# Kernel tuning notes

Hardware: AMD Instinct MI355X
Metric: run time of the kernel (lower is better)

## Reference

```python
import jax, jax.numpy as jnp
import numpy as np

N, T, NC, D = 256, 20, 1, 32
NF, Q, VSTEPS, HDYN = 16, 32, 10, 256
HDIM = NF * 64           # n_filt * 4**3
DT = 0.1
BETA = 1.0
LOG2PI = float(np.log(2.0 * np.pi))


def conv2d(x, w, b):
    # k=4, s=2, p=1 : halves spatial dims. x: [B,Cin,H,W], w: [Cout,Cin,4,4]
    y = jax.lax.conv_general_dilated(x, w, (2, 2), [(1, 1), (1, 1)],
                                     dimension_numbers=('NCHW', 'OIHW', 'NCHW'))
    return y + b[None, :, None, None]


def deconv2d(x, w, b):
    # stride-2 transposed conv, doubles spatial dims. w: [Cout,Cin,4,4]
    y = jax.lax.conv_transpose(x, w, (2, 2), 'SAME',
                               dimension_numbers=('NCHW', 'OIHW', 'NCHW'))
    return y + b[None, :, None, None]


def encode(x, C1, c1, C2, c2, C3, c3, Wm, bm, Wl, bl):
    h = jax.nn.relu(conv2d(x, C1, c1))
    h = jax.nn.relu(conv2d(h, C2, c2))
    h = jax.nn.relu(conv2d(h, C3, c3))   # [B, 4*NF, 4, 4]
    h = h.reshape(h.shape[0], -1)        # [B, HDIM]
    return h @ Wm + bm, h @ Wl + bl


def setup_inputs() -> dict:
    key = jax.random.key(0)
    ks = jax.random.split(key, 40)
    r = lambda i, shape, s=0.05: s * jax.random.normal(ks[i], shape, jnp.float32)
    inp = {
        'X': jax.random.uniform(ks[0], (N, T, NC, D, D), jnp.float32),
        'eps_s0': jax.random.normal(ks[1], (N, Q), jnp.float32),
        'eps_v0': jax.random.normal(ks[2], (N, Q), jnp.float32),
        # enc_s (input = 1 frame)
        'Cs1': r(3, (NF, NC, 4, 4)), 'cs1': jnp.zeros((NF,)),
        'Cs2': r(4, (2 * NF, NF, 4, 4)), 'cs2': jnp.zeros((2 * NF,)),
        'Cs3': r(5, (4 * NF, 2 * NF, 4, 4)), 'cs3': jnp.zeros((4 * NF,)),
        'Wsm': r(6, (HDIM, Q)), 'bsm': jnp.zeros((Q,)),
        'Wsl': r(7, (HDIM, Q), 0.01), 'bsl': -1.0 * jnp.ones((Q,)),
        # enc_v (input = v_steps frames stacked as channels)
        'Cv1': r(8, (NF, VSTEPS * NC, 4, 4)), 'cv1': jnp.zeros((NF,)),
        'Cv2': r(9, (2 * NF, NF, 4, 4)), 'cv2': jnp.zeros((2 * NF,)),
        'Cv3': r(10, (4 * NF, 2 * NF, 4, 4)), 'cv3': jnp.zeros((4 * NF,)),
        'Wvm': r(11, (HDIM, Q)), 'bvm': jnp.zeros((Q,)),
        'Wvl': r(12, (HDIM, Q), 0.01), 'bvl': -1.0 * jnp.ones((Q,)),
        # dynamics f : R^{2q} -> R^q (tanh MLP)
        'W1': r(13, (2 * Q, HDYN), 0.1), 'b1': jnp.zeros((HDYN,)),
        'W2': r(14, (HDYN, Q), 0.1), 'b2': jnp.zeros((Q,)),
        # fc3 + decoder
        'Wf': r(15, (Q, HDIM)), 'bf': jnp.zeros((HDIM,)),
        'D1': r(16, (2 * NF, 4 * NF, 4, 4)), 'd1': jnp.zeros((2 * NF,)),
        'D2': r(17, (NF, 2 * NF, 4, 4)), 'd2': jnp.zeros((NF,)),
        'D3': r(18, (NC, NF, 4, 4)), 'd3': jnp.zeros((NC,)),
        'Ndata': 10000,
    }
    return inp


def reference(X, eps_s0, eps_v0,
              Cs1, cs1, Cs2, cs2, Cs3, cs3, Wsm, bsm, Wsl, bsl,
              Cv1, cv1, Cv2, cv2, Cv3, cv3, Wvm, bvm, Wvl, bvl,
              W1, b1, W2, b2, Wf, bf, D1, d1, D2, d2, D3, d3, Ndata):
    Nb, Tt = X.shape[0], X.shape[1]
    # ---- encode z0 = [v0, s0]
    s0_mu, s0_lv = encode(X[:, 0], Cs1, cs1, Cs2, cs2, Cs3, cs3, Wsm, bsm, Wsl, bsl)
    xv = X[:, :VSTEPS].reshape(Nb, VSTEPS * NC, D, D)
    v0_mu, v0_lv = encode(xv, Cv1, cv1, Cv2, cv2, Cv3, cv3, Wvm, bvm, Wvl, bvl)
    s0 = s0_mu + eps_s0 * jnp.exp(s0_lv)
    v0 = v0_mu + eps_v0 * jnp.exp(v0_lv)
    # standard-normal density of the base noise (q dims each)
    logp0 = (-0.5 * jnp.sum(eps_s0 ** 2, -1) - 0.5 * Q * LOG2PI) + \
            (-0.5 * jnp.sum(eps_v0 ** 2, -1) - 0.5 * Q * LOG2PI)
    z0 = jnp.concatenate([v0, s0], axis=1)               # [N,2q]
    qz0_m = jnp.concatenate([v0_mu, s0_mu], axis=1)
    qz0_logv = jnp.concatenate([v0_lv, s0_lv], axis=1)

    # ---- augmented ODE rhs: dz = [f(z), v], dlogp = -tr(df/dv)
    # exact trace for the tanh MLP: J = W2^T diag(1-h^2) W1^T, so
    # tr_{i<q} J = (1-h^2) @ c with c_k = sum_{i<q} W1[i,k] * W2[k,i]
    c = jnp.sum(W1[:Q] * W2.T, axis=0)                   # [HDYN]

    def rhs(vs):
        h = jnp.tanh(vs @ W1 + b1)                       # [N,HDYN]
        dv = h @ W2 + b2                                 # [N,q]
        dvs = jnp.concatenate([dv, vs[:, :Q]], axis=1)   # [N,2q]
        tr = (1.0 - h * h) @ c                           # [N]
        return dvs, -tr

    def rk4_step(carry, _):
        z, lp = carry
        k1z, k1l = rhs(z)
        k2z, k2l = rhs(z + 0.5 * DT * k1z)
        k3z, k3l = rhs(z + 0.5 * DT * k2z)
        k4z, k4l = rhs(z + DT * k3z)
        z2 = z + (DT / 6.0) * (k1z + 2 * k2z + 2 * k3z + k4z)
        lp2 = lp + (DT / 6.0) * (k1l + 2 * k2l + 2 * k3l + k4l)
        return (z2, lp2), (z2, lp2)

    (_, _), (zs, lps) = jax.lax.scan(rk4_step, (z0, logp0), None, length=Tt - 1)
    zt = jnp.concatenate([z0[None], zs], axis=0)         # [T,N,2q]
    logp = jnp.concatenate([logp0[None], lps], axis=0)   # [T,N]
    ztL = jnp.transpose(zt, (1, 0, 2))[None]             # [1,N,T,2q] (L=1)
    logpL = logp.T[None]                                 # [1,N,T]

    # ---- decode positions s_t
    s = ztL[..., Q:].reshape(-1, Q) @ Wf + bf            # [N*T, HDIM]
    h = s.reshape(-1, 4 * NF, 4, 4)
    h = jax.nn.relu(deconv2d(h, D1, d1))                 # [N*T,2NF,8,8]
    h = jax.nn.relu(deconv2d(h, D2, d2))                 # [N*T,NF,16,16]
    Xrec = jax.nn.sigmoid(deconv2d(h, D3, d3))           # [N*T,NC,32,32]
    Xrec = Xrec.reshape(1, Nb, Tt, NC, D, D)

    # ---- ELBO
    log_pzt = -0.5 * jnp.sum(ztL ** 2, -1) - Q * LOG2PI  # N(0,I) over 2q dims
    kl_z = (logpL - log_pzt).sum(2).mean(0)              # [N]
    lhood_L = jnp.log(0.001 + Xrec) * X[None] + jnp.log(1.001 - Xrec) * (1.0 - X[None])
    lhood = lhood_L.sum((2, 3, 4, 5)).mean(0)            # [N]
    kl_w = 0.5 * (jnp.sum(W1 ** 2) + jnp.sum(W2 ** 2))
    Nd = jnp.float32(Ndata)
    lh = Nd * lhood.mean()
    klz = Nd * kl_z.mean()
    elbo = lh - klz - BETA * kl_w
    return Xrec, qz0_m, qz0_logv, ztL, elbo, lh, klz, BETA * kl_w


if __name__ == '__main__':
    outs = reference(**setup_inputs())
    print(outs[0].shape, float(outs[4]))
```

## Files before the change

kernel.cpp:

```cpp
#include <hip/hip_runtime.h>
#include <math.h>

#define N_S 256
#define T_S 20
#define D_S 32
#define NF_S 16
#define Q_S 32
#define HDYN_S 256
#define HDIM_S 1024
#define VSTEPS_S 10
#define DT_S 0.1f
#define LOG2PI_F 1.8378770664093453f

#define OUT_XREC 0
#define OUT_QM   5242880
#define OUT_QLV  5259264
#define OUT_ZT   5275648
#define OUT_SCAL 5603328

#define WS_A1    0
#define WS_A3    0
#define WS_A2    1048576
#define WS_S0MU  1572864
#define WS_S0LV  1581056
#define WS_V0MU  1589248
#define WS_V0LV  1597440
#define WS_LHOOD 1610752
#define WS_KLZ   1611008
#define WS_TC    1611520
#define TC_S1 (WS_TC + 0)
#define TC_V1 (WS_TC + 256)
#define TC_S2 (WS_TC + 2816)
#define TC_V2 (WS_TC + 11008)
#define TC_S3 (WS_TC + 19200)
#define TC_V3 (WS_TC + 51968)
#define WS_WT1   1703936
#define WS_WT2   1736704
#define WS_WT3   1744896
#define SC_A1S 0
#define SC_A2S 1048576
#define SC_A3S 1572864

__device__ inline void enc_tr(const float* __restrict__ src, float* __restrict__ dst,
                              int e, int CI, int CO) {
    int co = e % CO; int r = e / CO; int tap = r & 15; int ci = r >> 4;
    dst[e] = src[(co * CI + ci) * 16 + tap];
}
__device__ inline void dec_tr(const float* __restrict__ src, float* __restrict__ dst,
                              int e, int CI, int CO) {
    int co = e % CO; int r = e / CO; int ci = r % CI; int tap = r / CI;
    dst[e] = src[(co * CI + ci) * 16 + tap];
}

__global__ __launch_bounds__(256) void prep_all(
    const float* __restrict__ Cs1, const float* __restrict__ Cv1,
    const float* __restrict__ Cs2, const float* __restrict__ Cv2,
    const float* __restrict__ Cs3, const float* __restrict__ Cv3,
    const float* __restrict__ D1, const float* __restrict__ D2,
    const float* __restrict__ D3,
    float* __restrict__ ws)
{
    int idx = blockIdx.x * 256 + threadIdx.x;
    if (blockIdx.x == 0) ws[WS_LHOOD + threadIdx.x] = 0.f;
    if (idx < 256)        enc_tr(Cs1, ws + TC_S1, idx,          1, 16);
    else if (idx < 2816)  enc_tr(Cv1, ws + TC_V1, idx - 256,   10, 16);
    else if (idx < 11008) enc_tr(Cs2, ws + TC_S2, idx - 2816,  16, 32);
    else if (idx < 19200) enc_tr(Cv2, ws + TC_V2, idx - 11008, 16, 32);
    else if (idx < 51968) enc_tr(Cs3, ws + TC_S3, idx - 19200, 32, 64);
    else if (idx < 84736) enc_tr(Cv3, ws + TC_V3, idx - 51968, 32, 64);
    else if (idx < 117504) dec_tr(D1, ws + WS_WT1, idx - 84736,  64, 32);
    else if (idx < 125696) dec_tr(D2, ws + WS_WT2, idx - 117504, 32, 16);
    else if (idx < 125952) dec_tr(D3, ws + WS_WT3, idx - 125696, 16, 1);
}

__global__ __launch_bounds__(256) void conv1_both(
    const float* __restrict__ x,
    const float* __restrict__ wtS, const float* __restrict__ wtV,
    const float* __restrict__ bS, const float* __restrict__ bV,
    float* __restrict__ outS, float* __restrict__ outV)
{
    __shared__ float xin[10 * 630];
    __shared__ float wlv[10 * 256];
    __shared__ float wls[256];
    __shared__ float blv[16], bls[16];
    int b = blockIdx.x, yh = blockIdx.y, t = threadIdx.x;
    for (int e = t; e < 10 * 576; e += 256) {
        int ci = e / 576;
        int r = (e >> 5) - ci * 18;
        int cx = e & 31;
        int gy = yh * 16 - 1 + r;
        float v = (gy >= 0 && gy < 32) ? x[(size_t)b * 20480 + ci * 1024 + gy * 32 + cx] : 0.f;
        xin[ci * 630 + r * 35 + cx + 1] = v;
    }
    for (int e = t; e < 10 * 18; e += 256) {
        int ci = e / 18, r = e - ci * 18;
        xin[ci * 630 + r * 35 + 0] = 0.f;
        xin[ci * 630 + r * 35 + 33] = 0.f;
    }
    for (int e = t; e < 10 * 256; e += 256) wlv[e] = wtV[e];
    wls[t] = wtS[t];
    if (t < 16) { blv[t] = bV[t]; bls[t] = bS[t]; }
    __syncthreads();

    int ocq = t >> 7, p = t & 127;
    int oyl = p >> 4, ox = p & 15;
    float accv[8], accs[8];
    #pragma unroll
    for (int j = 0; j < 8; j++) { accv[j] = blv[ocq * 8 + j]; accs[j] = bls[ocq * 8 + j]; }
    for (int ci = 0; ci < 10; ci++) {
        const float* xc = xin + ci * 630;
        const float* wc = wlv + ci * 256 + ocq * 8;
        const float* wcs = wls + ocq * 8;
        bool do_s = (ci == 0);
        #pragma unroll
        for (int ky = 0; ky < 4; ky++) {
            const float* xr = xc + (2 * oyl + ky) * 35;
            #pragma unroll
            for (int kx = 0; kx < 4; kx++) {
                float v = xr[2 * ox + kx];
                const float4* w4 = (const float4*)(wc + (ky * 4 + kx) * 16);
                float4 wa = w4[0], wb = w4[1];
                accv[0] = fmaf(v, wa.x, accv[0]);
                accv[1] = fmaf(v, wa.y, accv[1]);
                accv[2] = fmaf(v, wa.z, accv[2]);
                accv[3] = fmaf(v, wa.w, accv[3]);
                accv[4] = fmaf(v, wb.x, accv[4]);
                accv[5] = fmaf(v, wb.y, accv[5]);
                accv[6] = fmaf(v, wb.z, accv[6]);
                accv[7] = fmaf(v, wb.w, accv[7]);
                if (do_s) {
                    const float4* s4 = (const float4*)(wcs + (ky * 4 + kx) * 16);
                    float4 sa = s4[0], sb = s4[1];
                    accs[0] = fmaf(v, sa.x, accs[0]);
                    accs[1] = fmaf(v, sa.y, accs[1]);
                    accs[2] = fmaf(v, sa.z, accs[2]);
                    accs[3] = fmaf(v, sa.w, accs[3]);
                    accs[4] = fmaf(v, sb.x, accs[4]);
                    accs[5] = fmaf(v, sb.y, accs[5]);
                    accs[6] = fmaf(v, sb.z, accs[6]);
                    accs[7] = fmaf(v, sb.w, accs[7]);
                }
            }
        }
    }
    int oy = yh * 8 + oyl;
    size_t ob = (size_t)b * 4096 + (size_t)(ocq * 8) * 256 + oy * 16 + ox;
    #pragma unroll
    for (int j = 0; j < 8; j++) {
        outV[ob + (size_t)j * 256] = fmaxf(accv[j], 0.f);
        outS[ob + (size_t)j * 256] = fmaxf(accs[j], 0.f);
    }
}

__global__ __launch_bounds__(256) void conv2_m(
    const float* __restrict__ a1S, const float* __restrict__ a1V,
    const float* __restrict__ wtS, const float* __restrict__ wtV,
    const float* __restrict__ bS, const float* __restrict__ bV,
    float* __restrict__ outS, float* __restrict__ outV)
{
    __shared__ float xin[16 * 272];
    __shared__ float wl[4096];
    __shared__ float bl[16];
    int b = blockIdx.x, h = blockIdx.y, z = blockIdx.z, t = threadIdx.x;
    const float* a1 = z ? a1V : a1S;
    const float* wt = z ? wtV : wtS;
    const float* bias = z ? bV : bS;
    float* out = z ? outV : outS;
    for (int e = t; e < 4096; e += 256) {
        int ci = e >> 8, r = e & 255, iy = r >> 4, ix = r & 15;
        xin[ci * 272 + iy * 17 + ix] = a1[(size_t)b * 4096 + e];
    }
    for (int e = t; e < 4096; e += 256) {
        int ci = e >> 8, r = e & 255, tap = r >> 4, oc = r & 15;
        wl[e] = wt[ci * 512 + tap * 32 + h * 16 + oc];
    }
    if (t < 16) bl[t] = bias[h * 16 + t];
    __syncthreads();

    int ocq = t >> 6, p = t & 63;
    int pa = p >> 3, pb = p & 7;
    float acc[4];
    #pragma unroll
    for (int j = 0; j < 4; j++) acc[j] = bl[ocq * 4 + j];
    for (int ci = 0; ci < 16; ci++) {
        const float* xc = xin + ci * 272;
        const float* wc = wl + ci * 256 + ocq * 4;
        #pragma unroll
        for (int ky = 0; ky < 4; ky++) {
            int iy = 2 * pa - 1 + ky;
            if ((unsigned)iy >= 16u) continue;
            const float* xr = xc + iy * 17;
            #pragma unroll
            for (int kx = 0; kx < 4; kx++) {
                int ix = 2 * pb - 1 + kx;
                if ((unsigned)ix >= 16u) continue;
                float v = xr[ix];
                float4 wv = *(const float4*)(wc + (ky * 4 + kx) * 16);
                acc[0] = fmaf(v, wv.x, acc[0]);
                acc[1] = fmaf(v, wv.y, acc[1]);
                acc[2] = fmaf(v, wv.z, acc[2]);
                acc[3] = fmaf(v, wv.w, acc[3]);
            }
        }
    }
    size_t ob = (size_t)b * 2048 + (size_t)(h * 16 + ocq * 4) * 64 + pa * 8 + pb;
    #pragma unroll
    for (int j = 0; j < 4; j++) out[ob + (size_t)j * 64] = fmaxf(acc[j], 0.f);
}

__global__ __launch_bounds__(256) void conv3_m(
    const float* __restrict__ a2S, const float* __restrict__ a2V,
    const float* __restrict__ wtS, const float* __restrict__ wtV,
    const float* __restrict__ bS, const float* __restrict__ bV,
    float* __restrict__ outS, float* __restrict__ outV)
{
    __shared__ float xin[32 * 72];
    __shared__ float wl[8192];
    __shared__ float bl[16];
    int b = blockIdx.x, h = blockIdx.y, z = blockIdx.z, t = threadIdx.x;
    const float* a2 = z ? a2V : a2S;
    const float* wt = z ? wtV : wtS;
    const float* bias = z ? bV : bS;
    float* out = z ? outV : outS;
    for (int e = t; e < 2048; e += 256) {
        int ci = e >> 6, r = e & 63, iy = r >> 3, ix = r & 7;
        xin[ci * 72 + iy * 9 + ix] = a2[(size_t)b * 2048 + e];
    }
    for (int e = t; e < 8192; e += 256) {
        int ci = e >> 8, r = e & 255, tap = r >> 4, oc = r & 15;
        wl[e] = wt[ci * 1024 + tap * 64 + h * 16 + oc];
    }
    if (t < 16) bl[t] = bias[h * 16 + t];
    __syncthreads();

    int oc = t >> 4, p = t & 15;
    int pa = p >> 2, pb = p & 3;
    float s0 = bl[oc], s1 = 0.f;
    for (int ci = 0; ci < 32; ci += 2) {
        const float* xc0 = xin + ci * 72;
        const float* wc0 = wl + ci * 256 + oc;
        #pragma unroll
        for (int ky = 0; ky < 4; ky++) {
            int iy = 2 * pa - 1 + ky;
            if ((unsigned)iy >= 8u) continue;
            const float* xr0 = xc0 + iy * 9;
            #pragma unroll
            for (int kx = 0; kx < 4; kx++) {
                int ix = 2 * pb - 1 + kx;
                if ((unsigned)ix >= 8u) continue;
                int wi = (ky * 4 + kx) * 16;
                s0 = fmaf(xr0[ix],      wc0[wi],       s0);
                s1 = fmaf(xr0[72 + ix], wc0[256 + wi], s1);
            }
        }
    }
    out[(size_t)b * 1024 + h * 256 + t] = fmaxf(s0 + s1, 0.f);
}

__global__ __launch_bounds__(256) void fc_m(
    const float* __restrict__ hS, const float* __restrict__ hV,
    const float* __restrict__ WsmP, const float* __restrict__ bsmP,
    const float* __restrict__ WslP, const float* __restrict__ bslP,
    const float* __restrict__ WvmP, const float* __restrict__ bvmP,
    const float* __restrict__ WvlP, const float* __restrict__ bvlP,
    float* __restrict__ muS, float* __restrict__ lvS,
    float* __restrict__ muV, float* __restrict__ lvV)
{
    __shared__ float pm[8][32], pl[8][32];
    int b = blockIdx.x, z = blockIdx.y, t = threadIdx.x;
    const float* h  = z ? hV : hS;
    const float* Wm = z ? WvmP : WsmP;
    const float* Wl = z ? WvlP : WslP;
    const float* bm = z ? bvmP : bsmP;
    const float* bl = z ? bvlP : bslP;
    float* mu = z ? muV : muS;
    float* lv = z ? lvV : lvS;
    int q = t & 31, c = t >> 5;
    const float* hb = h + (size_t)b * HDIM_S + c * 128;
    const float* wmp = Wm + (c * 128) * Q_S + q;
    const float* wlp = Wl + (c * 128) * Q_S + q;
    float am = 0.f, al = 0.f;
    #pragma unroll 4
    for (int k = 0; k < 128; k++) {
        float hv = hb[k];
        am = fmaf(hv, wmp[k * Q_S], am);
        al = fmaf(hv, wlp[k * Q_S], al);
    }
    pm[c][q] = am; pl[c][q] = al;
    __syncthreads();
    if (t < 32) {
        float s = bm[t];
        #pragma unroll
        for (int c2 = 0; c2 < 8; c2++) s += pm[c2][t];
        mu[b * Q_S + t] = s;
    } else if (t < 64) {
        int qq = t - 32;
        float s = bl[qq];
        #pragma unroll
        for (int c2 = 0; c2 < 8; c2++) s += pl[c2][qq];
        lv[b * Q_S + qq] = s;
    }
}

__global__ __launch_bounds__(256) void ode2(
    const float* __restrict__ W1, const float* __restrict__ b1,
    const float* __restrict__ W2, const float* __restrict__ b2,
    const float* __restrict__ s0mu, const float* __restrict__ s0lv,
    const float* __restrict__ v0mu, const float* __restrict__ v0lv,
    const float* __restrict__ eps_s, const float* __restrict__ eps_v,
    float* __restrict__ qm, float* __restrict__ qlv,
    float* __restrict__ ztL, float* __restrict__ klz)
{
    __shared__ float W2s[HDYN_S * Q_S];
    __shared__ float zeval[64];
    __shared__ float hsh[HDYN_S];
    __shared__ float dvred[HDYN_S];
    __shared__ float red4[4];
    int n = blockIdx.x;
    int t = threadIdx.x;

    for (int i = t; i < HDYN_S * Q_S; i += 256) W2s[i] = W2[i];
    float w1r[64];
    #pragma unroll
    for (int j = 0; j < 64; j++) w1r[j] = W1[j * HDYN_S + t];
    float b1r = b1[t];

    size_t zoff = (size_t)n * T_S * 64;
    float zj = 0.f, zevalj = 0.f, lp = 0.f, klzacc = 0.f;
    float ep = 0.f;
    if (t < 64) {
        int q = t & 31;
        float mu, lvv;
        if (t < 32) { mu = v0mu[n*32+q]; lvv = v0lv[n*32+q]; ep = eps_v[n*32+q]; }
        else        { mu = s0mu[n*32+q]; lvv = s0lv[n*32+q]; ep = eps_s[n*32+q]; }
        zj = fmaf(ep, expf(lvv), mu);
        qm[n*64 + t]  = mu;
        qlv[n*64 + t] = lvv;
        ztL[zoff + t] = zj;
        zevalj = zj; zeval[t] = zj;
        float e2 = ep * ep;
        float z2 = zj * zj;
        #pragma unroll
        for (int off = 32; off; off >>= 1) {
            e2 += __shfl_down(e2, off, 64);
            z2 += __shfl_down(z2, off, 64);
        }
        if (t == 0) {
            lp = -0.5f * e2 - Q_S * LOG2PI_F;
            klzacc = lp + 0.5f * z2 + Q_S * LOG2PI_F;
        }
    }
    __syncthreads();
    float ck = 0.f;
    #pragma unroll
    for (int i = 0; i < Q_S; i++) ck = fmaf(w1r[i], W2s[t * Q_S + i], ck);

    float ksumj = 0.f, lsum = 0.f;
    const float wc[4] = {1.f, 2.f, 2.f, 1.f};
    const float ac[3] = {0.5f * DT_S, 0.5f * DT_S, DT_S};

    for (int step = 1; step < T_S; step++) {
        for (int e = 0; e < 4; e++) {
            __syncthreads();
            float p0 = 0.f, p1 = 0.f, p2 = 0.f, p3 = 0.f;
            const float4* ze4 = (const float4*)zeval;
            #pragma unroll
            for (int jj = 0; jj < 4; jj++) {
                float4 za = ze4[jj], zb = ze4[jj + 4], zc = ze4[jj + 8], zd = ze4[jj + 12];
                p0 = fmaf(za.x, w1r[jj*4+0], p0);
                p0 = fmaf(za.y, w1r[jj*4+1], p0);
                p0 = fmaf(za.z, w1r[jj*4+2], p0);
                p0 = fmaf(za.w, w1r[jj*4+3], p0);
                p1 = fmaf(zb.x, w1r[16+jj*4+0], p1);
                p1 = fmaf(zb.y, w1r[16+jj*4+1], p1);
                p1 = fmaf(zb.z, w1r[16+jj*4+2], p1);
                p1 = fmaf(zb.w, w1r[16+jj*4+3], p1);
                p2 = fmaf(zc.x, w1r[32+jj*4+0], p2);
                p2 = fmaf(zc.y, w1r[32+jj*4+1], p2);
                p2 = fmaf(zc.z, w1r[32+jj*4+2], p2);
                p2 = fmaf(zc.w, w1r[32+jj*4+3], p2);
                p3 = fmaf(zd.x, w1r[48+jj*4+0], p3);
                p3 = fmaf(zd.y, w1r[48+jj*4+1], p3);
                p3 = fmaf(zd.z, w1r[48+jj*4+2], p3);
                p3 = fmaf(zd.w, w1r[48+jj*4+3], p3);
            }
            float pre = b1r + ((p0 + p1) + (p2 + p3));
            float hk = tanhf(pre);
            hsh[t] = hk;
            float gk = (1.f - hk * hk) * ck;
            #pragma unroll
            for (int off = 32; off; off >>= 1) gk += __shfl_down(gk, off, 64);
            if ((t & 63) == 0) red4[t >> 6] = gk;
            __syncthreads();
            {
                int i = t & 31, p = t >> 5;
                const float4* h4 = (const float4*)(hsh + p * 32);
                const float* wbase = W2s + (p * 32) * Q_S + i;
                float a0 = 0.f, a1 = 0.f;
                #pragma unroll
                for (int k4 = 0; k4 < 4; k4++) {
                    float4 ha = h4[k4], hb = h4[k4 + 4];
                    const float* wk = wbase + k4 * 4 * Q_S;
                    a0 = fmaf(ha.x, wk[0],        a0);
                    a0 = fmaf(ha.y, wk[Q_S],      a0);
                    a0 = fmaf(ha.z, wk[2*Q_S],    a0);
                    a0 = fmaf(ha.w, wk[3*Q_S],    a0);
                    const float* wk2 = wbase + (16 + k4 * 4) * Q_S;
                    a1 = fmaf(hb.x, wk2[0],       a1);
                    a1 = fmaf(hb.y, wk2[Q_S],     a1);
                    a1 = fmaf(hb.z, wk2[2*Q_S],   a1);
                    a1 = fmaf(hb.w, wk2[3*Q_S],   a1);
                }
                dvred[t] = a0 + a1;
            }
            __syncthreads();
            if (t < 64) {
                float tr = red4[0] + red4[1] + red4[2] + red4[3];
                float zv_shfl = __shfl(zevalj, (t >= 32) ? (t - 32) : t, 64);
                float kzv;
                if (t < 32) {
                    float dvi = b2[t];
                    #pragma unroll
                    for (int p = 0; p < 8; p++) dvi += dvred[p * 32 + t];
                    kzv = dvi;
                } else kzv = zv_shfl;
                if (e == 0) ksumj = kzv; else ksumj = fmaf(wc[e], kzv, ksumj);
                if (t == 0) { float kl = -tr; lsum = (e == 0) ? kl : fmaf(wc[e], kl, lsum); }
                if (e < 3) {
                    zevalj = fmaf(ac[e], kzv, zj);
                    zeval[t] = zevalj;
                } else {
                    zj = fmaf(DT_S / 6.f, ksumj, zj);
                    zevalj = zj; zeval[t] = zj;
                    ztL[zoff + step * 64 + t] = zj;
                    float e2z = zj * zj;
                    #pragma unroll
                    for (int off = 32; off; off >>= 1) e2z += __shfl_down(e2z, off, 64);
                    if (t == 0) {
                        lp = fmaf(DT_S / 6.f, lsum, lp);
                        klzacc += lp + 0.5f * e2z + Q_S * LOG2PI_F;
                    }
                }
            }
        }
    }
    if (t == 0) klz[n] = klzacc;
}

__global__ __launch_bounds__(256) void decoder9(
    const float* __restrict__ ztL, const float* __restrict__ Wf, const float* __restrict__ bf,
    const float* __restrict__ wt1, const float* __restrict__ d1,
    const float* __restrict__ wt2, const float* __restrict__ d2,
    const float* __restrict__ wt3, const float* __restrict__ d3,
    const float* __restrict__ X, float* __restrict__ Xrec, float* __restrict__ lhood)
{
    __shared__ float zs[32];
    __shared__ float h1s[2404];
    __shared__ float u2[5332];
    __shared__ float sh4[4];
    float* slp = u2;
    float* h2p = u2;
    float* xst = h1s;
    const int bidx = blockIdx.x;
    const int t = threadIdx.x;
    const int wu = __builtin_amdgcn_readfirstlane(t >> 6);
    const int l = t & 63;
    const int py = wu >> 1, px = wu & 1;

    if (t < 32) zs[t] = ztL[(size_t)bidx * 64 + 32 + t];
    if (t < 68) u2[5264 + t] = 0.f;
    if (t < 36) h1s[2368 + t] = 0.f;
    __syncthreads();

    {
        float4 acc = ((const float4*)bf)[t];
        const float4* Wf4 = (const float4*)Wf;
        #pragma unroll 4
        for (int q = 0; q < 32; q++) {
            float zq = zs[q];
            float4 wv = Wf4[q * 256 + t];
            acc.x = fmaf(zq, wv.x, acc.x);
            acc.y = fmaf(zq, wv.y, acc.y);
            acc.z = fmaf(zq, wv.z, acc.z);
            acc.w = fmaf(zq, wv.w, acc.w);
        }
        int ci = t >> 2;
        int iy = t & 3;
        float vv[4] = {acc.x, acc.y, acc.z, acc.w};
        #pragma unroll
        for (int j = 0; j < 4; j++)
            slp[iy * 276 + j * 68 + ci] = vv[j];
    }
    __syncthreads();

    {
        int ocq = l >> 3;
        int pp = l & 7;
        int a_ = pp >> 1, b2 = pp & 1;
        float acc0[4], acc1[4];
        #pragma unroll
        for (int j = 0; j < 4; j++) { acc0[j] = d1[ocq * 4 + j]; acc1[j] = acc0[j]; }
        #pragma unroll
        for (int sy = 0; sy < 2; sy++) {
            int ky = py + 2 * sy;
            int iy = a_ + py + sy - 1;
            bool rowok = (unsigned)iy < 4u;
            #pragma unroll
            for (int sx = 0; sx < 2; sx++) {
                int kx = px + 2 * sx;
                int ix0 = 2 * b2 + px + sx - 1;
                int ix1 = ix0 + 1;
                int off0 = (rowok && (unsigned)ix0 < 4u) ? (iy * 276 + ix0 * 68) : 5264;
                int off1 = (rowok && (unsigned)ix1 < 4u) ? (iy * 276 + ix1 * 68) : 5264;
                const float4* ip0 = (const float4*)(u2 + off0);
                const float4* ip1 = (const float4*)(u2 + off1);
                const float* wb = wt1 + (ky * 4 + kx) * 2048 + ocq * 4;
                #pragma unroll 4
                for (int cc = 0; cc < 16; cc++) {
                    float4 va = ip0[cc];
                    float4 vb = ip1[cc];
                    float av[4] = {va.x, va.y, va.z, va.w};
                    float bv[4] = {vb.x, vb.y, vb.z, vb.w};
                    #pragma unroll
                    for (int r = 0; r < 4; r++) {
                        float4 wv = *(const float4*)(wb + (cc * 4 + r) * 32);
                        acc0[0] = fmaf(av[r], wv.x, acc0[0]); acc1[0] = fmaf(bv[r], wv.x, acc1[0]);
                        acc0[1] = fmaf(av[r], wv.y, acc0[1]); acc1[1] = fmaf(bv[r], wv.y, acc1[1]);
                        acc0[2] = fmaf(av[r], wv.z, acc0[2]); acc1[2] = fmaf(bv[r], wv.z, acc1[2]);
                        acc0[3] = fmaf(av[r], wv.w, acc0[3]); acc1[3] = fmaf(bv[r], wv.w, acc1[3]);
                    }
                }
            }
        }
        float* hp = h1s + (py * 2 + px) * 592;
        int ox0 = 2 * b2, ox1 = ox0 + 1;
        float4 r0, r1;
        r0.x = fmaxf(acc0[0],0.f); r0.y = fmaxf(acc0[1],0.f); r0.z = fmaxf(acc0[2],0.f); r0.w = fmaxf(acc0[3],0.f);
        r1.x = fmaxf(acc1[0],0.f); r1.y = fmaxf(acc1[1],0.f); r1.z = fmaxf(acc1[2],0.f); r1.w = fmaxf(acc1[3],0.f);
        *(float4*)(hp + a_ * 148 + ox0 * 36 + ocq * 4) = r0;
        *(float4*)(hp + a_ * 148 + ox1 * 36 + ocq * 4) = r1;
    }
    __syncthreads();

    {
        int a = l >> 3, b = l & 7;
        float acc[16];
        #pragma unroll
        for (int j = 0; j < 16; j++) acc[j] = d2[j];
        #pragma unroll
        for (int sy = 0; sy < 2; sy++) {
            int ky = py + 2 * sy;
            int iyf = a + py + sy - 1;
            int pyi = iyf & 1, ly = iyf >> 1;
            bool yok = (unsigned)iyf < 8u;
            #pragma unroll
            for (int sx = 0; sx < 2; sx++) {
                int kx = px + 2 * sx;
                int ixf = b + px + sx - 1;
                int pxi = ixf & 1, lx = ixf >> 1;
                int off = (yok && (unsigned)ixf < 8u)
                          ? ((pyi * 2 + pxi) * 592 + ly * 148 + lx * 36) : 2368;
                const float4* ip4 = (const float4*)(h1s + off);
                const float* wb = wt2 + (ky * 4 + kx) * 512;
                #pragma unroll 2
                for (int cc = 0; cc < 8; cc++) {
                    float4 v = ip4[cc];
                    float vv[4] = {v.x, v.y, v.z, v.w};
                    #pragma unroll
                    for (int r = 0; r < 4; r++) {
                        const float4* wq = (const float4*)(wb + (cc * 4 + r) * 16);
                        float4 w0 = wq[0], w1 = wq[1], w2 = wq[2], w3 = wq[3];
                        float vr = vv[r];
                        acc[0]  = fmaf(vr, w0.x, acc[0]);
                        acc[1]  = fmaf(vr, w0.y, acc[1]);
                        acc[2]  = fmaf(vr, w0.z, acc[2]);
                        acc[3]  = fmaf(vr, w0.w, acc[3]);
                        acc[4]  = fmaf(vr, w1.x, acc[4]);
                        acc[5]  = fmaf(vr, w1.y, acc[5]);
                        acc[6]  = fmaf(vr, w1.z, acc[6]);
                        acc[7]  = fmaf(vr, w1.w, acc[7]);
                        acc[8]  = fmaf(vr, w2.x, acc[8]);
                        acc[9]  = fmaf(vr, w2.y, acc[9]);
                        acc[10] = fmaf(vr, w2.z, acc[10]);
                        acc[11] = fmaf(vr, w2.w, acc[11]);
                        acc[12] = fmaf(vr, w3.x, acc[12]);
                        acc[13] = fmaf(vr, w3.y, acc[13]);
                        acc[14] = fmaf(vr, w3.z, acc[14]);
                        acc[15] = fmaf(vr, w3.w, acc[15]);
                    }
                }
            }
        }
        float* hq = h2p + (py * 2 + px) * 1316 + a * 164 + b * 20;
        #pragma unroll
        for (int j = 0; j < 4; j++) {
            float4 r;
            r.x = fmaxf(acc[j*4+0], 0.f);
            r.y = fmaxf(acc[j*4+1], 0.f);
            r.z = fmaxf(acc[j*4+2], 0.f);
            r.w = fmaxf(acc[j*4+3], 0.f);
            *(float4*)(hq + j * 4) = r;
        }
    }
    __syncthreads();

    {
        int u = l >> 3, v = l & 7;
        int ib = 2 * u + py - 1;
        int jb = 2 * v + px - 1;
        int offp[3][3];
        #pragma unroll
        for (int r = 0; r < 3; r++) {
            int iy = ib + r;
            int pyi = iy & 1, ly = iy >> 1;
            bool yok = (unsigned)iy < 16u;
            #pragma unroll
            for (int c = 0; c < 3; c++) {
                int ix = jb + c;
                int pxi = ix & 1, lx = ix >> 1;
                offp[r][c] = (yok && (unsigned)ix < 16u)
                             ? ((pyi * 2 + pxi) * 1316 + ly * 164 + lx * 20) : 5264;
            }
        }
        float d30 = d3[0];
        float acc[4] = {d30, d30, d30, d30};
        #pragma unroll
        for (int cc = 0; cc < 4; cc++) {
            float4 pix[3][3];
            #pragma unroll
            for (int r = 0; r < 3; r++)
                #pragma unroll
                for (int c = 0; c < 3; c++)
                    pix[r][c] = ((const float4*)(u2 + offp[r][c]))[cc];
            #pragma unroll
            for (int sy = 0; sy < 2; sy++) {
                int ky = py + 2 * sy;
                #pragma unroll
                for (int sx = 0; sx < 2; sx++) {
                    int kx = px + 2 * sx;
                    float4 wq = ((const float4*)(wt3 + (ky * 4 + kx) * 16))[cc];
                    #pragma unroll
                    for (int dy = 0; dy < 2; dy++) {
                        #pragma unroll
                        for (int dx = 0; dx < 2; dx++) {
                            float4 p4 = pix[dy + sy][dx + sx];
                            float s = acc[dy * 2 + dx];
                            s = fmaf(p4.x, wq.x, s);
                            s = fmaf(p4.y, wq.y, s);
                            s = fmaf(p4.z, wq.z, s);
                            s = fmaf(p4.w, wq.w, s);
                            acc[dy * 2 + dx] = s;
                        }
                    }
                }
            }
        }
        #pragma unroll
        for (int dy = 0; dy < 2; dy++) {
            #pragma unroll
            for (int dx = 0; dx < 2; dx++) {
                int oy = 4 * u + 2 * dy + py;
                int ox = 4 * v + 2 * dx + px;
                xst[oy * 36 + ox] = 1.f / (1.f + expf(-acc[dy * 2 + dx]));
            }
        }
    }
    __syncthreads();

    {
        int row = t >> 3, col = (t & 7) * 4;
        float4 xr4 = *(const float4*)(xst + row * 36 + col);
        *(float4*)(Xrec + (size_t)bidx * 1024 + t * 4) = xr4;
        float4 xi4 = *(const float4*)(X + (size_t)bidx * 1024 + t * 4);
        float ll = 0.f;
        ll += logf(0.001f + xr4.x) * xi4.x + logf(1.001f - xr4.x) * (1.f - xi4.x);
        ll += logf(0.001f + xr4.y) * xi4.y + logf(1.001f - xr4.y) * (1.f - xi4.y);
        ll += logf(0.001f + xr4.z) * xi4.z + logf(1.001f - xr4.z) * (1.f - xi4.z);
        ll += logf(0.001f + xr4.w) * xi4.w + logf(1.001f - xr4.w) * (1.f - xi4.w);
        #pragma unroll
        for (int off = 32; off; off >>= 1) ll += __shfl_down(ll, off, 64);
        if ((t & 63) == 0) sh4[t >> 6] = ll;
    }
    __syncthreads();
    if (t == 0) atomicAdd(&lhood[bidx / T_S], sh4[0] + sh4[1] + sh4[2] + sh4[3]);
}

__global__ __launch_bounds__(256) void final2(
    const float* __restrict__ lhood, const float* __restrict__ klz,
    const float* __restrict__ W1, const float* __restrict__ W2,
    const int* __restrict__ Ndata, float* __restrict__ outs)
{
    __shared__ float shA[4], shB[4], shC[4];
    int t = threadIdx.x;
    float a = lhood[t];
    float b = klz[t];
    float c = 0.f;
    for (int i = t; i < 64 * HDYN_S; i += 256) c = fmaf(W1[i], W1[i], c);
    for (int i = t; i < HDYN_S * Q_S; i += 256) c = fmaf(W2[i], W2[i], c);
    #pragma unroll
    for (int off = 32; off; off >>= 1) {
        a += __shfl_down(a, off, 64);
        b += __shfl_down(b, off, 64);
        c += __shfl_down(c, off, 64);
    }
    if ((t & 63) == 0) { shA[t >> 6] = a; shB[t >> 6] = b; shC[t >> 6] = c; }
    __syncthreads();
    if (t == 0) {
        float Nd = (float)Ndata[0];
        float lh = Nd * ((shA[0] + shA[1] + shA[2] + shA[3]) / 256.f);
        float kz = Nd * ((shB[0] + shB[1] + shB[2] + shB[3]) / 256.f);
        float bkw = 0.5f * (shC[0] + shC[1] + shC[2] + shC[3]);
        outs[0] = lh - kz - bkw;
        outs[1] = lh;
        outs[2] = kz;
        outs[3] = bkw;
    }
}

extern "C" void kernel_launch(void* const* d_in, const int* in_sizes, int n_in,
                              void* d_out, int out_size, void* d_ws, size_t ws_size,
                              hipStream_t stream) {
    const float* X      = (const float*)d_in[0];
    const float* eps_s0 = (const float*)d_in[1];
    const float* eps_v0 = (const float*)d_in[2];
    const float* Cs1 = (const float*)d_in[3],  *cs1 = (const float*)d_in[4];
    const float* Cs2 = (const float*)d_in[5],  *cs2 = (const float*)d_in[6];
    const float* Cs3 = (const float*)d_in[7],  *cs3 = (const float*)d_in[8];
    const float* Wsm = (const float*)d_in[9],  *bsm = (const float*)d_in[10];
    const float* Wsl = (const float*)d_in[11], *bsl = (const float*)d_in[12];
    const float* Cv1 = (const float*)d_in[13], *cv1 = (const float*)d_in[14];
    const float* Cv2 = (const float*)d_in[15], *cv2 = (const float*)d_in[16];
    const float* Cv3 = (const float*)d_in[17], *cv3 = (const float*)d_in[18];
    const float* Wvm = (const float*)d_in[19], *bvm = (const float*)d_in[20];
    const float* Wvl = (const float*)d_in[21], *bvl = (const float*)d_in[22];
    const float* W1  = (const float*)d_in[23], *b1  = (const float*)d_in[24];
    const float* W2  = (const float*)d_in[25], *b2  = (const float*)d_in[26];
    const float* Wf  = (const float*)d_in[27], *bf  = (const float*)d_in[28];
    const float* D1  = (const float*)d_in[29], *d1  = (const float*)d_in[30];
    const float* D2  = (const float*)d_in[31], *d2  = (const float*)d_in[32];
    const float* D3  = (const float*)d_in[33], *d3  = (const float*)d_in[34];
    const int*   Ndata = (const int*)d_in[35];

    float* out = (float*)d_out;
    float* ws  = (float*)d_ws;
    float* scr = out + OUT_XREC;

    prep_all<<<492, 256, 0, stream>>>(Cs1, Cv1, Cs2, Cv2, Cs3, Cv3, D1, D2, D3, ws);

    conv1_both<<<dim3(256, 2), 256, 0, stream>>>(X, ws + TC_S1, ws + TC_V1, cs1, cv1,
                                                 scr + SC_A1S, ws + WS_A1);

    conv2_m<<<dim3(256, 2, 2), 256, 0, stream>>>(scr + SC_A1S, ws + WS_A1,
                                                 ws + TC_S2, ws + TC_V2, cs2, cv2,
                                                 scr + SC_A2S, ws + WS_A2);
    conv3_m<<<dim3(256, 4, 2), 256, 0, stream>>>(scr + SC_A2S, ws + WS_A2,
                                                 ws + TC_S3, ws + TC_V3, cs3, cv3,
                                                 scr + SC_A3S, ws + WS_A3);
    fc_m<<<dim3(256, 2), 256, 0, stream>>>(scr + SC_A3S, ws + WS_A3,
                                           Wsm, bsm, Wsl, bsl, Wvm, bvm, Wvl, bvl,
                                           ws + WS_S0MU, ws + WS_S0LV,
                                           ws + WS_V0MU, ws + WS_V0LV);

    ode2<<<256, 256, 0, stream>>>(W1, b1, W2, b2,
                                  ws + WS_S0MU, ws + WS_S0LV, ws + WS_V0MU, ws + WS_V0LV,
                                  eps_s0, eps_v0,
                                  out + OUT_QM, out + OUT_QLV,
                                  out + OUT_ZT, ws + WS_KLZ);

    decoder9<<<5120, 256, 0, stream>>>(out + OUT_ZT, Wf, bf,
                                       ws + WS_WT1, d1, ws + WS_WT2, d2, ws + WS_WT3, d3,
                                       X, out + OUT_XREC, ws + WS_LHOOD);

    final2<<<1, 256, 0, stream>>>(ws + WS_LHOOD, ws + WS_KLZ, W1, W2, Ndata,
                                  out + OUT_SCAL);
}
```

Before: 586.3 us.

## Split conv1 into four row blocks and pack two images per decoder block

conv1_both now launches four row-quarter blocks per image, each thread computing 4 output channels instead of 8. This doubles parallelism and cuts the shared-memory input tile per block. The decoder now processes two images per 512-thread block with duplicated shared buffers, halving the number of blocks and atomics. The lhood atomic index becomes blockIdx/10, which relies on T=20 being even so a block's two images share a sample. The trade-off is higher shared memory per decoder block, which may lower occupancy, and more redundant halo loads in conv1.

After: 662.0 us. 12.9% more time.

```diff
diff --git a/kernel.cpp b/kernel.cpp
--- a/kernel.cpp
+++ b/kernel.cpp
@@ -79,38 +79,39 @@
     const float* __restrict__ bS, const float* __restrict__ bV,
     float* __restrict__ outS, float* __restrict__ outV)
 {
-    __shared__ float xin[10 * 630];
+    __shared__ float xin[10 * 350];
     __shared__ float wlv[10 * 256];
     __shared__ float wls[256];
     __shared__ float blv[16], bls[16];
-    int b = blockIdx.x, yh = blockIdx.y, t = threadIdx.x;
-    for (int e = t; e < 10 * 576; e += 256) {
-        int ci = e / 576;
-        int r = (e >> 5) - ci * 18;
+    int b = blockIdx.x, yq = blockIdx.y, t = threadIdx.x;
+    for (int e = t; e < 3200; e += 256) {
+        int ci = e / 320;
+        int r = (e >> 5) - ci * 10;
         int cx = e & 31;
-        int gy = yh * 16 - 1 + r;
+        int gy = yq * 8 - 1 + r;
         float v = (gy >= 0 && gy < 32) ? x[(size_t)b * 20480 + ci * 1024 + gy * 32 + cx] : 0.f;
-        xin[ci * 630 + r * 35 + cx + 1] = v;
-    }
-    for (int e = t; e < 10 * 18; e += 256) {
-        int ci = e / 18, r = e - ci * 18;
-        xin[ci * 630 + r * 35 + 0] = 0.f;
-        xin[ci * 630 + r * 35 + 33] = 0.f;
-    }
-    for (int e = t; e < 10 * 256; e += 256) wlv[e] = wtV[e];
+        xin[ci * 350 + r * 35 + cx + 1] = v;
+    }
+    for (int e = t; e < 100; e += 256) {
+        int ci = e / 10, r = e - ci * 10;
+        xin[ci * 350 + r * 35 + 0] = 0.f;
+        xin[ci * 350 + r * 35 + 33] = 0.f;
+    }
+    for (int e = t; e < 2560; e += 256) wlv[e] = wtV[e];
     wls[t] = wtS[t];
     if (t < 16) { blv[t] = bV[t]; bls[t] = bS[t]; }
     __syncthreads();
 
-    int ocq = t >> 7, p = t & 127;
+    int ocq = t >> 6;
+    int p = t & 63;
     int oyl = p >> 4, ox = p & 15;
-    float accv[8], accs[8];
+    float accv[4], accs[4];
     #pragma unroll
-    for (int j = 0; j < 8; j++) { accv[j] = blv[ocq * 8 + j]; accs[j] = bls[ocq * 8 + j]; }
+    for (int j = 0; j < 4; j++) { accv[j] = blv[ocq * 4 + j]; accs[j] = bls[ocq * 4 + j]; }
     for (int ci = 0; ci < 10; ci++) {
-        const float* xc = xin + ci * 630;
-        const float* wc = wlv + ci * 256 + ocq * 8;
-        const float* wcs = wls + ocq * 8;
+        const float* xc = xin + ci * 350;
+        const float* wc = wlv + ci * 256 + ocq * 4;
+        const float* wcs = wls + ocq * 4;
         bool do_s = (ci == 0);
         #pragma unroll
         for (int ky = 0; ky < 4; ky++) {
@@ -118,35 +119,25 @@
             #pragma unroll
             for (int kx = 0; kx < 4; kx++) {
                 float v = xr[2 * ox + kx];
-                const float4* w4 = (const float4*)(wc + (ky * 4 + kx) * 16);
-                float4 wa = w4[0], wb = w4[1];
-                accv[0] = fmaf(v, wa.x, accv[0]);
-                accv[1] = fmaf(v, wa.y, accv[1]);
-                accv[2] = fmaf(v, wa.z, accv[2]);
-                accv[3] = fmaf(v, wa.w, accv[3]);
-                accv[4] = fmaf(v, wb.x, accv[4]);
-                accv[5] = fmaf(v, wb.y, accv[5]);
-                accv[6] = fmaf(v, wb.z, accv[6]);
-                accv[7] = fmaf(v, wb.w, accv[7]);
+                float4 wv = *(const float4*)(wc + (ky * 4 + kx) * 16);
+                accv[0] = fmaf(v, wv.x, accv[0]);
+                accv[1] = fmaf(v, wv.y, accv[1]);
+                accv[2] = fmaf(v, wv.z, accv[2]);
+                accv[3] = fmaf(v, wv.w, accv[3]);
                 if (do_s) {
-                    const float4* s4 = (const float4*)(wcs + (ky * 4 + kx) * 16);
-                    float4 sa = s4[0], sb = s4[1];
-                    accs[0] = fmaf(v, sa.x, accs[0]);
-                    accs[1] = fmaf(v, sa.y, accs[1]);
-                    accs[2] = fmaf(v, sa.z, accs[2]);
-                    accs[3] = fmaf(v, sa.w, accs[3]);
-                    accs[4] = fmaf(v, sb.x, accs[4]);
-                    accs[5] = fmaf(v, sb.y, accs[5]);
-                    accs[6] = fmaf(v, sb.z, accs[6]);
-                    accs[7] = fmaf(v, sb.w, accs[7]);
+                    float4 sv = *(const float4*)(wcs + (ky * 4 + kx) * 16);
+                    accs[0] = fmaf(v, sv.x, accs[0]);
+                    accs[1] = fmaf(v, sv.y, accs[1]);
+                    accs[2] = fmaf(v, sv.z, accs[2]);
+                    accs[3] = fmaf(v, sv.w, accs[3]);
                 }
             }
         }
     }
-    int oy = yh * 8 + oyl;
-    size_t ob = (size_t)b * 4096 + (size_t)(ocq * 8) * 256 + oy * 16 + ox;
+    int oy = yq * 4 + oyl;
+    size_t ob = (size_t)b * 4096 + (size_t)(ocq * 4) * 256 + oy * 16 + ox;
     #pragma unroll
-    for (int j = 0; j < 8; j++) {
+    for (int j = 0; j < 4; j++) {
         outV[ob + (size_t)j * 256] = fmaxf(accv[j], 0.f);
         outS[ob + (size_t)j * 256] = fmaxf(accs[j], 0.f);
     }
@@ -447,49 +438,52 @@
     if (t == 0) klz[n] = klzacc;
 }
 
-__global__ __launch_bounds__(256) void decoder9(
+__global__ __launch_bounds__(512) void decoder10(
     const float* __restrict__ ztL, const float* __restrict__ Wf, const float* __restrict__ bf,
     const float* __restrict__ wt1, const float* __restrict__ d1,
     const float* __restrict__ wt2, const float* __restrict__ d2,
     const float* __restrict__ wt3, const float* __restrict__ d3,
     const float* __restrict__ X, float* __restrict__ Xrec, float* __restrict__ lhood)
 {
-    __shared__ float zs[32];
-    __shared__ float h1s[2404];
-    __shared__ float u2[5332];
-    __shared__ float sh4[4];
-    float* slp = u2;
-    float* h2p = u2;
-    float* xst = h1s;
-    const int bidx = blockIdx.x;
+    __shared__ float zs[64];
+    __shared__ float h1a[2][2404];
+    __shared__ float u2a[2][5332];
+    __shared__ float sh8[8];
     const int t = threadIdx.x;
-    const int wu = __builtin_amdgcn_readfirstlane(t >> 6);
+    const int img = t >> 8;
+    const int tl = t & 255;
+    const int wu = __builtin_amdgcn_readfirstlane((t >> 6) & 3);
     const int l = t & 63;
     const int py = wu >> 1, px = wu & 1;
-
-    if (t < 32) zs[t] = ztL[(size_t)bidx * 64 + 32 + t];
-    if (t < 68) u2[5264 + t] = 0.f;
-    if (t < 36) h1s[2368 + t] = 0.f;
+    const int bimg = blockIdx.x * 2 + img;
+    float* u2i = u2a[img];
+    float* h1i = h1a[img];
+    float* xst = h1i;
+
+    if (tl < 32) zs[img * 32 + tl] = ztL[(size_t)bimg * 64 + 32 + tl];
+    if (tl < 68) u2i[5264 + tl] = 0.f;
+    if (tl < 36) h1i[2368 + tl] = 0.f;
     __syncthreads();
 
     {
-        float4 acc = ((const float4*)bf)[t];
+        float4 acc = ((const float4*)bf)[tl];
         const float4* Wf4 = (const float4*)Wf;
+        const float* zsi = zs + img * 32;
         #pragma unroll 4
         for (int q = 0; q < 32; q++) {
-            float zq = zs[q];
-            float4 wv = Wf4[q * 256 + t];
+            float zq = zsi[q];
+            float4 wv = Wf4[q * 256 + tl];
             acc.x = fmaf(zq, wv.x, acc.x);
             acc.y = fmaf(zq, wv.y, acc.y);
             acc.z = fmaf(zq, wv.z, acc.z);
             acc.w = fmaf(zq, wv.w, acc.w);
         }
-        int ci = t >> 2;
-        int iy = t & 3;
+        int ci = tl >> 2;
+        int iy = tl & 3;
         float vv[4] = {acc.x, acc.y, acc.z, acc.w};
         #pragma unroll
         for (int j = 0; j < 4; j++)
-            slp[iy * 276 + j * 68 + ci] = vv[j];
+            u2i[iy * 276 + j * 68 + ci] = vv[j];
     }
     __syncthreads();
 
@@ -512,8 +506,8 @@
                 int ix1 = ix0 + 1;
                 int off0 = (rowok && (unsigned)ix0 < 4u) ? (iy * 276 + ix0 * 68) : 5264;
                 int off1 = (rowok && (unsigned)ix1 < 4u) ? (iy * 276 + ix1 * 68) : 5264;
-                const float4* ip0 = (const float4*)(u2 + off0);
-                const float4* ip1 = (const float4*)(u2 + off1);
+                const float4* ip0 = (const float4*)(u2i + off0);
+                const float4* ip1 = (const float4*)(u2i + off1);
                 const float* wb = wt1 + (ky * 4 + kx) * 2048 + ocq * 4;
                 #pragma unroll 4
                 for (int cc = 0; cc < 16; cc++) {
@@ -532,7 +526,7 @@
                 }
             }
         }
-        float* hp = h1s + (py * 2 + px) * 592;
+        float* hp = h1i + (py * 2 + px) * 592;
         int ox0 = 2 * b2, ox1 = ox0 + 1;
         float4 r0, r1;
         r0.x = fmaxf(acc0[0],0.f); r0.y = fmaxf(acc0[1],0.f); r0.z = fmaxf(acc0[2],0.f); r0.w = fmaxf(acc0[3],0.f);
@@ -560,7 +554,7 @@
                 int pxi = ixf & 1, lx = ixf >> 1;
                 int off = (yok && (unsigned)ixf < 8u)
                           ? ((pyi * 2 + pxi) * 592 + ly * 148 + lx * 36) : 2368;
-                const float4* ip4 = (const float4*)(h1s + off);
+                const float4* ip4 = (const float4*)(h1i + off);
                 const float* wb = wt2 + (ky * 4 + kx) * 512;
                 #pragma unroll 2
                 for (int cc = 0; cc < 8; cc++) {
@@ -591,7 +585,7 @@
                 }
             }
         }
-        float* hq = h2p + (py * 2 + px) * 1316 + a * 164 + b * 20;
+        float* hq = u2i + (py * 2 + px) * 1316 + a * 164 + b * 20;
         #pragma unroll
         for (int j = 0; j < 4; j++) {
             float4 r;
@@ -631,7 +625,7 @@
             for (int r = 0; r < 3; r++)
                 #pragma unroll
                 for (int c = 0; c < 3; c++)
-                    pix[r][c] = ((const float4*)(u2 + offp[r][c]))[cc];
+                    pix[r][c] = ((const float4*)(u2i + offp[r][c]))[cc];
             #pragma unroll
             for (int sy = 0; sy < 2; sy++) {
                 int ky = py + 2 * sy;
@@ -668,10 +662,10 @@
     __syncthreads();
 
     {
-        int row = t >> 3, col = (t & 7) * 4;
+        int row = tl >> 3, col = (tl & 7) * 4;
         float4 xr4 = *(const float4*)(xst + row * 36 + col);
-        *(float4*)(Xrec + (size_t)bidx * 1024 + t * 4) = xr4;
-        float4 xi4 = *(const float4*)(X + (size_t)bidx * 1024 + t * 4);
+        *(float4*)(Xrec + (size_t)bimg * 1024 + tl * 4) = xr4;
+        float4 xi4 = *(const float4*)(X + (size_t)bimg * 1024 + tl * 4);
         float ll = 0.f;
         ll += logf(0.001f + xr4.x) * xi4.x + logf(1.001f - xr4.x) * (1.f - xi4.x);
         ll += logf(0.001f + xr4.y) * xi4.y + logf(1.001f - xr4.y) * (1.f - xi4.y);
@@ -679,10 +673,14 @@
         ll += logf(0.001f + xr4.w) * xi4.w + logf(1.001f - xr4.w) * (1.f - xi4.w);
         #pragma unroll
         for (int off = 32; off; off >>= 1) ll += __shfl_down(ll, off, 64);
-        if ((t & 63) == 0) sh4[t >> 6] = ll;
-    }
-    __syncthreads();
-    if (t == 0) atomicAdd(&lhood[bidx / T_S], sh4[0] + sh4[1] + sh4[2] + sh4[3]);
+        if (l == 0) sh8[t >> 6] = ll;
+    }
+    __syncthreads();
+    if (t == 0) {
+        float tot = sh8[0] + sh8[1] + sh8[2] + sh8[3]
+                  + sh8[4] + sh8[5] + sh8[6] + sh8[7];
+        atomicAdd(&lhood[blockIdx.x / 10], tot);
+    }
 }
 
 __global__ __launch_bounds__(256) void final2(
@@ -747,7 +745,7 @@
 
     prep_all<<<492, 256, 0, stream>>>(Cs1, Cv1, Cs2, Cv2, Cs3, Cv3, D1, D2, D3, ws);
 
-    conv1_both<<<dim3(256, 2), 256, 0, stream>>>(X, ws + TC_S1, ws + TC_V1, cs1, cv1,
+    conv1_both<<<dim3(256, 4), 256, 0, stream>>>(X, ws + TC_S1, ws + TC_V1, cs1, cv1,
                                                  scr + SC_A1S, ws + WS_A1);
 
     conv2_m<<<dim3(256, 2, 2), 256, 0, stream>>>(scr + SC_A1S, ws + WS_A1,
@@ -767,9 +765,9 @@
                                   out + OUT_QM, out + OUT_QLV,
                                   out + OUT_ZT, ws + WS_KLZ);
 
-    decoder9<<<5120, 256, 0, stream>>>(out + OUT_ZT, Wf, bf,
-                                       ws + WS_WT1, d1, ws + WS_WT2, d2, ws + WS_WT3, d3,
-                                       X, out + OUT_XREC, ws + WS_LHOOD);
+    decoder10<<<2560, 512, 0, stream>>>(out + OUT_ZT, Wf, bf,
+                                        ws + WS_WT1, d1, ws + WS_WT2, d2, ws + WS_WT3, d3,
+                                        X, out + OUT_XREC, ws + WS_LHOOD);
 
     final2<<<1, 256, 0, stream>>>(ws + WS_LHOOD, ws + WS_KLZ, W1, W2, Ndata,
                                   out + OUT_SCAL);
```
